# Performance work log

Hardware: AMD Instinct MI355X
Metric: run time of the kernel (lower is better)

Reference implementation:

```python
import jax, jax.numpy as jnp
import numpy as np

K_INIT = 16  # self.k from __init__

def setup_inputs() -> dict:
    key = jax.random.key(0)
    center = jax.random.normal(key, (8192, 64), dtype=jnp.float32)
    return {"center": center}

def _cdist(x):
    # Euclidean pairwise distances, matmul-based like torch.cdist(p=2).
    x2 = jnp.sum(x * x, axis=-1)  # [N]
    d2 = x2[:, None] + x2[None, :] - 2.0 * (x @ x.T)  # [N, N]
    d2 = jnp.maximum(d2, 0.0)
    # safe sqrt (grad-safe at 0; forward identical)
    d = jnp.sqrt(jnp.where(d2 > 0.0, d2, 1.0))
    return jnp.where(d2 > 0.0, d, 0.0)

def reference(center):
    n, d_feat = center.shape
    k = min(K_INIT + 1, d_feat)  # faithful to torch: min(self.k + 1, center.shape[1])
    dist = _cdist(center)  # [N, N]
    # smallest-k via top_k on negated distances
    _, indices = jax.lax.top_k(-dist, k)  # [N, k]
    neighbor_indices = indices[:, 1:]  # drop self, [N, k-1]
    mean_dists = jnp.take_along_axis(dist, neighbor_indices, axis=1).mean(axis=1)  # [N]
    logp = jax.nn.log_softmax(mean_dists, axis=0)  # = softmax(mean_dists).log()
    q = 1.0 / n
    # F.kl_div(p.log(), q, reduction='sum') = sum q * (log q - log p)
    loss = jnp.sum(q * (jnp.log(jnp.float32(q)) - logp))
    return loss
```

## Files before the change

kernel.cpp:

```cpp
#include <hip/hip_runtime.h>
#include <hip/hip_bf16.h>
#include <math.h>

#define N_PTS 8192
#define D_FEAT 64
#define KP 128
#define TPB 512
#define ROWS_B 32
#define JSPLIT 2
#define JRANGE (N_PTS / JSPLIT)
#define CHUNKS_PB (JRANGE / 32)
#define PASSES (CHUNKS_PB / 8)
#define NLIST 32

typedef __attribute__((ext_vector_type(8))) short short8v;
typedef __attribute__((ext_vector_type(16))) float f32x16;

__device__ ushort g_X2[N_PTS * KP];
__device__ float  g_x2n[N_PTS];
__device__ float  g_part[(size_t)N_PTS * NLIST * 16];
__device__ float  g_md[N_PTS];

__global__ __launch_bounds__(256) void pack_kernel(const float* __restrict__ x) {
    const int row = blockIdx.x * 256 + threadIdx.x;
    const int chunk = row >> 5, r = row & 31;
    const float4* xr = (const float4*)(x + (size_t)row * D_FEAT);
    ushort* base = g_X2 + (size_t)chunk * 4096 + r * 8;
    float norm = 0.f;
    #pragma unroll
    for (int it = 0; it < 8; ++it) {
        float4 a = xr[2 * it], b = xr[2 * it + 1];
        float vals[8] = {a.x, a.y, a.z, a.w, b.x, b.y, b.z, b.w};
        uint hi[8], lo[8];
        #pragma unroll
        for (int e = 0; e < 8; ++e) {
            float v = vals[e];
            norm += v * v;
            uint u = __float_as_uint(v);
            uint rh = (u + 0x7fffu + ((u >> 16) & 1u)) >> 16;
            hi[e] = rh;
            float l = v - __uint_as_float(rh << 16);
            uint u2 = __float_as_uint(l);
            lo[e] = (u2 + 0x7fffu + ((u2 >> 16) & 1u)) >> 16;
        }
        *(uint4*)(base + it * 256) = make_uint4(
            hi[0] | (hi[1] << 16), hi[2] | (hi[3] << 16),
            hi[4] | (hi[5] << 16), hi[6] | (hi[7] << 16));
        *(uint4*)(base + (8 + it) * 256) = make_uint4(
            lo[0] | (lo[1] << 16), lo[2] | (lo[3] << 16),
            lo[4] | (lo[5] << 16), lo[6] | (lo[7] << 16));
    }
    g_x2n[row] = norm;
}

#define CE(A, B) { float lo_ = fminf(A, B); float hi_ = fmaxf(A, B); A = lo_; B = hi_; }

__global__ __launch_bounds__(TPB, 3) void nn_kernel() {
    __shared__ float s_x2[JRANGE];
    const int t    = threadIdx.x;
    const int lane = t & 63;
    const int w    = t >> 6;
    const int il   = lane & 31;
    const int h    = lane >> 5;
    const int ib   = blockIdx.x >> 1;
    const int jslice = blockIdx.x & 1;
    const int i0   = ib * ROWS_B;
    const int c0   = jslice * CHUNKS_PB;
    const float INF = __builtin_inff();

    {
        float4* s4 = (float4*)s_x2;
        const float4* g4 = (const float4*)(g_x2n + jslice * JRANGE);
        #pragma unroll
        for (int q = 0; q < 2; ++q) s4[t + q * TPB] = g4[t + q * TPB];
    }

    const short8v* Xf = (const short8v*)g_X2;

    short8v bfr[8];
    {
        const short8v* bp = Xf + (size_t)(ib * 16 + h) * 32 + il;
        #pragma unroll
        for (int tt = 0; tt < 8; ++tt) bfr[tt] = bp[(size_t)(2 * tt) * 32];
    }
    __syncthreads();

    float t16[16];
    #pragma unroll
    for (int k = 0; k < 16; ++k) t16[k] = INF;

    const short8v* abase = Xf + (size_t)((c0 + w) * 16 + h) * 32 + il;
    #define ALOAD(dst, p) { \
        const short8v* ab_ = abase + (size_t)(p) * 8 * 16 * 32; \
        _Pragma("unroll") \
        for (int tt = 0; tt < 8; ++tt) dst[tt] = ab_[(size_t)(2 * tt) * 32]; }

    #define EPILOG(accv, p) { \
        const int cl_ = (p) * 8 + w; \
        float c[16]; \
        _Pragma("unroll") \
        for (int g = 0; g < 4; ++g) { \
            float4 xq = *(const float4*)&s_x2[cl_ * 32 + 8 * g + 4 * h]; \
            float cand[4] = {xq.x, xq.y, xq.z, xq.w}; \
            _Pragma("unroll") \
            for (int e = 0; e < 4; ++e) \
                c[4 * g + e] = fmaf(-2.f, accv[4 * g + e], cand[e]); \
        } \
         \
        CE(c[0],c[8]) CE(c[1],c[9]) CE(c[2],c[10]) CE(c[3],c[11]) \
        CE(c[4],c[12]) CE(c[5],c[13]) CE(c[6],c[14]) CE(c[7],c[15]) \
        CE(c[0],c[4]) CE(c[1],c[5]) CE(c[2],c[6]) CE(c[3],c[7]) \
        CE(c[8],c[12]) CE(c[9],c[13]) CE(c[10],c[14]) CE(c[11],c[15]) \
        CE(c[4],c[8]) CE(c[5],c[9]) CE(c[6],c[10]) CE(c[7],c[11]) \
        CE(c[0],c[2]) CE(c[1],c[3]) CE(c[4],c[6]) CE(c[5],c[7]) \
        CE(c[8],c[10]) CE(c[9],c[11]) CE(c[12],c[14]) CE(c[13],c[15]) \
        CE(c[2],c[8]) CE(c[3],c[9]) CE(c[6],c[12]) CE(c[7],c[13]) \
        CE(c[2],c[4]) CE(c[3],c[5]) CE(c[6],c[8]) CE(c[7],c[9]) \
        CE(c[10],c[12]) CE(c[11],c[13]) \
        CE(c[0],c[1]) CE(c[2],c[3]) CE(c[4],c[5]) CE(c[6],c[7]) \
        CE(c[8],c[9]) CE(c[10],c[11]) CE(c[12],c[13]) CE(c[14],c[15]) \
        CE(c[1],c[8]) CE(c[3],c[10]) CE(c[5],c[12]) CE(c[7],c[14]) \
        CE(c[1],c[4]) CE(c[3],c[6]) CE(c[5],c[8]) CE(c[7],c[10]) \
        CE(c[9],c[12]) CE(c[11],c[14]) \
        CE(c[1],c[2]) CE(c[3],c[4]) CE(c[5],c[6]) CE(c[7],c[8]) \
        CE(c[9],c[10]) CE(c[11],c[12]) CE(c[13],c[14]) \
         \
        _Pragma("unroll") \
        for (int i = 0; i < 16; ++i) t16[i] = fminf(t16[i], c[15 - i]); \
        _Pragma("unroll") \
        for (int j = 8; j > 0; j >>= 1) { \
            _Pragma("unroll") \
            for (int i = 0; i < 16; ++i) { \
                const int ix = i ^ j; \
                if (ix > i) { \
                    float lo = fminf(t16[i], t16[ix]); \
                    float hi = fmaxf(t16[i], t16[ix]); \
                    t16[i] = lo; \
                    t16[ix] = hi; \
                } \
            } \
        } }

    #define MFMA8(accv, areg) { \
        _Pragma("unroll") \
        for (int r = 0; r < 16; ++r) accv[r] = 0.f; \
        _Pragma("unroll") \
        for (int tt = 0; tt < 8; ++tt) \
            accv = __builtin_amdgcn_mfma_f32_32x32x16_bf16(areg[tt], bfr[tt], accv, 0, 0, 0); }

    short8v a0[8], a1[8];
    f32x16 acc;
    ALOAD(a0, 0);
    #pragma unroll 1
    for (int pp = 0; pp < PASSES / 2; ++pp) {
        const int p0 = 2 * pp, p1 = 2 * pp + 1;
        ALOAD(a1, p1);
        MFMA8(acc, a0);
        EPILOG(acc, p0);
        if (pp < PASSES / 2 - 1) ALOAD(a0, p1 + 1);
        MFMA8(acc, a1);
        EPILOG(acc, p1);
    }

    {
        const bool own = ((ib >> 7) == jslice) && (w == (ib & 7)) &&
                         (h == ((il >> 2) & 1));
        if (own) {
            #pragma unroll
            for (int k = 0; k < 15; ++k) t16[k] = t16[k + 1];
            t16[15] = INF;
        }
    }

    {
        const int list = jslice * 16 + w * 2 + h;
        const int row = i0 + il;
        float* dst = &g_part[((size_t)row * NLIST + list) * 16];
        *(float4*)(dst + 0)  = make_float4(t16[0],  t16[1],  t16[2],  t16[3]);
        *(float4*)(dst + 4)  = make_float4(t16[4],  t16[5],  t16[6],  t16[7]);
        *(float4*)(dst + 8)  = make_float4(t16[8],  t16[9],  t16[10], t16[11]);
        *(float4*)(dst + 12) = make_float4(t16[12], t16[13], t16[14], t16[15]);
    }
}

__global__ __launch_bounds__(512) void merge_kernel() {
    const int t = threadIdx.x, lane = t & 63, w = t >> 6;
    const int half = lane >> 5;
    const int sl = lane & 31;
    const int row = blockIdx.x * 16 + w * 2 + half;
    const float INF = __builtin_inff();

    float tl[16];
    {
        const float* src = &g_part[((size_t)row * NLIST + sl) * 16];
        float4 q0 = *(const float4*)(src + 0);
        float4 q1 = *(const float4*)(src + 4);
        float4 q2 = *(const float4*)(src + 8);
        float4 q3 = *(const float4*)(src + 12);
        tl[0] = q0.x;  tl[1] = q0.y;  tl[2] = q0.z;  tl[3] = q0.w;
        tl[4] = q1.x;  tl[5] = q1.y;  tl[6] = q1.z;  tl[7] = q1.w;
        tl[8] = q2.x;  tl[9] = q2.y;  tl[10] = q2.z; tl[11] = q2.w;
        tl[12] = q3.x; tl[13] = q3.y; tl[14] = q3.z; tl[15] = q3.w;
    }

    const float x2r = g_x2n[row];
    float sum = 0.f;
    #pragma unroll 1
    for (int it = 0; it < 16; ++it) {
        float m = tl[0]; int src = sl;
        #pragma unroll
        for (int off = 16; off > 0; off >>= 1) {
            float om = __shfl_xor(m, off);
            int os = __shfl_xor(src, off);
            if (om < m || (om == m && os < src)) { m = om; src = os; }
        }
        sum += sqrtf(fmaxf(m + x2r, 0.f));
        const bool pop = (sl == src);
        #pragma unroll
        for (int k = 0; k < 15; ++k) tl[k] = pop ? tl[k + 1] : tl[k];
        tl[15] = pop ? INF : tl[15];
    }
    if (sl == 0) g_md[row] = sum * (1.f / 16.f);
}

__global__ __launch_bounds__(1024) void loss_kernel(float* __restrict__ out) {
    __shared__ float s[1024];
    const int t = threadIdx.x;

    float m = -__builtin_inff();
    for (int j = t; j < N_PTS; j += 1024) m = fmaxf(m, g_md[j]);
    s[t] = m; __syncthreads();
    for (int off = 512; off > 0; off >>= 1) {
        if (t < off) s[t] = fmaxf(s[t], s[t + off]);
        __syncthreads();
    }
    m = s[0]; __syncthreads();

    float se = 0.f, sm = 0.f;
    for (int j = t; j < N_PTS; j += 1024) {
        float v = g_md[j];
        se += expf(v - m);
        sm += v;
    }
    s[t] = se; __syncthreads();
    for (int off = 512; off > 0; off >>= 1) {
        if (t < off) s[t] += s[t + off];
        __syncthreads();
    }
    float S = s[0]; __syncthreads();
    s[t] = sm; __syncthreads();
    for (int off = 512; off > 0; off >>= 1) {
        if (t < off) s[t] += s[t + off];
        __syncthreads();
    }
    float M = s[0];

    if (t == 0) {
        const float n = (float)N_PTS;
        out[0] = -logf(n) - M / n + (m + logf(S));
    }
}

extern "C" void kernel_launch(void* const* d_in, const int* in_sizes, int n_in,
                              void* d_out, int out_size, void* d_ws, size_t ws_size,
                              hipStream_t stream) {
    const float* x = (const float*)d_in[0];
    float* out = (float*)d_out;

    pack_kernel<<<N_PTS / 256, 256, 0, stream>>>(x);
    nn_kernel<<<(N_PTS / ROWS_B) * JSPLIT, TPB, 0, stream>>>();
    merge_kernel<<<N_PTS / 16, 512, 0, stream>>>();
    loss_kernel<<<1, 1024, 0, stream>>>(out);
}
```

Before: 67.60 us.

## Fuse top-k merge into nn kernel and drop the column split

The two-way column split and the separate merge kernel are removed. Each block now scans all 8192 columns, writes its 16 partial lists per row into shared memory, and merges them in-kernel with 16-lane shuffles. This removes the 8 MB global partial buffer round trip and one launch. The MFMA/epilogue loop is also reordered with two accumulators so one MFMA batch overlaps the previous epilogue. The cost is half as many blocks (256), which is fewer than two per CU, plus occupancy launch bounds lowered from 3 to 2, so latency hiding may suffer.

```diff
diff --git a/kernel.cpp b/kernel.cpp
--- a/kernel.cpp
+++ b/kernel.cpp
@@ -7,18 +7,14 @@
 #define KP 128
 #define TPB 512
 #define ROWS_B 32
-#define JSPLIT 2
-#define JRANGE (N_PTS / JSPLIT)
-#define CHUNKS_PB (JRANGE / 32)
-#define PASSES (CHUNKS_PB / 8)
-#define NLIST 32
+#define PASSES 32
+#define LSTRIDE 260
 
 typedef __attribute__((ext_vector_type(8))) short short8v;
 typedef __attribute__((ext_vector_type(16))) float f32x16;
 
 __device__ ushort g_X2[N_PTS * KP];
 __device__ float  g_x2n[N_PTS];
-__device__ float  g_part[(size_t)N_PTS * NLIST * 16];
 __device__ float  g_md[N_PTS];
 
 __global__ __launch_bounds__(256) void pack_kernel(const float* __restrict__ x) {
@@ -55,24 +51,22 @@
 
 #define CE(A, B) { float lo_ = fminf(A, B); float hi_ = fmaxf(A, B); A = lo_; B = hi_; }
 
-__global__ __launch_bounds__(TPB, 3) void nn_kernel() {
-    __shared__ float s_x2[JRANGE];
+__global__ __launch_bounds__(TPB, 2) void nn_kernel() {
+    __shared__ float s_mem[8320];
     const int t    = threadIdx.x;
     const int lane = t & 63;
     const int w    = t >> 6;
     const int il   = lane & 31;
     const int h    = lane >> 5;
-    const int ib   = blockIdx.x >> 1;
-    const int jslice = blockIdx.x & 1;
+    const int ib   = blockIdx.x;
     const int i0   = ib * ROWS_B;
-    const int c0   = jslice * CHUNKS_PB;
     const float INF = __builtin_inff();
 
     {
-        float4* s4 = (float4*)s_x2;
-        const float4* g4 = (const float4*)(g_x2n + jslice * JRANGE);
+        float4* s4 = (float4*)s_mem;
+        const float4* g4 = (const float4*)g_x2n;
         #pragma unroll
-        for (int q = 0; q < 2; ++q) s4[t + q * TPB] = g4[t + q * TPB];
+        for (int q = 0; q < 4; ++q) s4[t + q * TPB] = g4[t + q * TPB];
     }
 
     const short8v* Xf = (const short8v*)g_X2;
@@ -89,9 +83,9 @@
     #pragma unroll
     for (int k = 0; k < 16; ++k) t16[k] = INF;
 
-    const short8v* abase = Xf + (size_t)((c0 + w) * 16 + h) * 32 + il;
+    const short8v* abase = Xf + (size_t)(w * 16 + h) * 32 + il;
     #define ALOAD(dst, p) { \
-        const short8v* ab_ = abase + (size_t)(p) * 8 * 16 * 32; \
+        const short8v* ab_ = abase + (size_t)(p) * 4096; \
         _Pragma("unroll") \
         for (int tt = 0; tt < 8; ++tt) dst[tt] = ab_[(size_t)(2 * tt) * 32]; }
 
@@ -100,7 +94,7 @@
         float c[16]; \
         _Pragma("unroll") \
         for (int g = 0; g < 4; ++g) { \
-            float4 xq = *(const float4*)&s_x2[cl_ * 32 + 8 * g + 4 * h]; \
+            float4 xq = *(const float4*)&s_mem[cl_ * 32 + 8 * g + 4 * h]; \
             float cand[4] = {xq.x, xq.y, xq.z, xq.w}; \
             _Pragma("unroll") \
             for (int e = 0; e < 4; ++e) \
@@ -149,22 +143,22 @@
             accv = __builtin_amdgcn_mfma_f32_32x32x16_bf16(areg[tt], bfr[tt], accv, 0, 0, 0); }
 
     short8v a0[8], a1[8];
-    f32x16 acc;
+    f32x16 accA, accB;
     ALOAD(a0, 0);
+    MFMA8(accA, a0);
+    ALOAD(a1, 1);
     #pragma unroll 1
     for (int pp = 0; pp < PASSES / 2; ++pp) {
         const int p0 = 2 * pp, p1 = 2 * pp + 1;
-        ALOAD(a1, p1);
-        MFMA8(acc, a0);
-        EPILOG(acc, p0);
-        if (pp < PASSES / 2 - 1) ALOAD(a0, p1 + 1);
-        MFMA8(acc, a1);
-        EPILOG(acc, p1);
-    }
-
-    {
-        const bool own = ((ib >> 7) == jslice) && (w == (ib & 7)) &&
-                         (h == ((il >> 2) & 1));
+        MFMA8(accB, a1);
+        if (pp < PASSES / 2 - 1) ALOAD(a0, p0 + 2);
+        EPILOG(accA, p0);
+        if (pp < PASSES / 2 - 1) { ALOAD(a1, p1 + 2); MFMA8(accA, a0); }
+        EPILOG(accB, p1);
+    }
+
+    {
+        const bool own = (w == (ib & 7)) && (h == ((il >> 2) & 1));
         if (own) {
             #pragma unroll
             for (int k = 0; k < 15; ++k) t16[k] = t16[k + 1];
@@ -172,55 +166,53 @@
         }
     }
 
-    {
-        const int list = jslice * 16 + w * 2 + h;
-        const int row = i0 + il;
-        float* dst = &g_part[((size_t)row * NLIST + list) * 16];
+    __syncthreads();
+    {
+        const int list = w * 2 + h;
+        float* dst = &s_mem[il * LSTRIDE + list * 16];
         *(float4*)(dst + 0)  = make_float4(t16[0],  t16[1],  t16[2],  t16[3]);
         *(float4*)(dst + 4)  = make_float4(t16[4],  t16[5],  t16[6],  t16[7]);
         *(float4*)(dst + 8)  = make_float4(t16[8],  t16[9],  t16[10], t16[11]);
         *(float4*)(dst + 12) = make_float4(t16[12], t16[13], t16[14], t16[15]);
     }
-}
-
-__global__ __launch_bounds__(512) void merge_kernel() {
-    const int t = threadIdx.x, lane = t & 63, w = t >> 6;
-    const int half = lane >> 5;
-    const int sl = lane & 31;
-    const int row = blockIdx.x * 16 + w * 2 + half;
-    const float INF = __builtin_inff();
-
-    float tl[16];
-    {
-        const float* src = &g_part[((size_t)row * NLIST + sl) * 16];
-        float4 q0 = *(const float4*)(src + 0);
-        float4 q1 = *(const float4*)(src + 4);
-        float4 q2 = *(const float4*)(src + 8);
-        float4 q3 = *(const float4*)(src + 12);
-        tl[0] = q0.x;  tl[1] = q0.y;  tl[2] = q0.z;  tl[3] = q0.w;
-        tl[4] = q1.x;  tl[5] = q1.y;  tl[6] = q1.z;  tl[7] = q1.w;
-        tl[8] = q2.x;  tl[9] = q2.y;  tl[10] = q2.z; tl[11] = q2.w;
-        tl[12] = q3.x; tl[13] = q3.y; tl[14] = q3.z; tl[15] = q3.w;
-    }
-
-    const float x2r = g_x2n[row];
-    float sum = 0.f;
-    #pragma unroll 1
-    for (int it = 0; it < 16; ++it) {
-        float m = tl[0]; int src = sl;
-        #pragma unroll
-        for (int off = 16; off > 0; off >>= 1) {
-            float om = __shfl_xor(m, off);
-            int os = __shfl_xor(src, off);
-            if (om < m || (om == m && os < src)) { m = om; src = os; }
-        }
-        sum += sqrtf(fmaxf(m + x2r, 0.f));
-        const bool pop = (sl == src);
-        #pragma unroll
-        for (int k = 0; k < 15; ++k) tl[k] = pop ? tl[k + 1] : tl[k];
-        tl[15] = pop ? INF : tl[15];
-    }
-    if (sl == 0) g_md[row] = sum * (1.f / 16.f);
+    __syncthreads();
+
+    {
+        const int q  = lane >> 4;
+        const int sl = lane & 15;
+        const int r  = w * 4 + q;
+        const int row = i0 + r;
+        float tl[16];
+        {
+            const float* src = &s_mem[r * LSTRIDE + sl * 16];
+            float4 q0 = *(const float4*)(src + 0);
+            float4 q1 = *(const float4*)(src + 4);
+            float4 q2 = *(const float4*)(src + 8);
+            float4 q3 = *(const float4*)(src + 12);
+            tl[0]=q0.x; tl[1]=q0.y; tl[2]=q0.z; tl[3]=q0.w;
+            tl[4]=q1.x; tl[5]=q1.y; tl[6]=q1.z; tl[7]=q1.w;
+            tl[8]=q2.x; tl[9]=q2.y; tl[10]=q2.z; tl[11]=q2.w;
+            tl[12]=q3.x; tl[13]=q3.y; tl[14]=q3.z; tl[15]=q3.w;
+        }
+        const float x2r = g_x2n[row];
+        float sum = 0.f;
+        #pragma unroll 1
+        for (int it = 0; it < 16; ++it) {
+            float m = tl[0]; int src = sl;
+            #pragma unroll
+            for (int off = 8; off > 0; off >>= 1) {
+                float om = __shfl_xor(m, off);
+                int os = __shfl_xor(src, off);
+                if (om < m || (om == m && os < src)) { m = om; src = os; }
+            }
+            sum += sqrtf(fmaxf(m + x2r, 0.f));
+            const bool pop = (sl == src);
+            #pragma unroll
+            for (int k = 0; k < 15; ++k) tl[k] = pop ? tl[k + 1] : tl[k];
+            tl[15] = pop ? INF : tl[15];
+        }
+        if (sl == 0) g_md[row] = sum * (1.f / 16.f);
+    }
 }
 
 __global__ __launch_bounds__(1024) void loss_kernel(float* __restrict__ out) {
@@ -268,7 +260,6 @@
     float* out = (float*)d_out;
 
     pack_kernel<<<N_PTS / 256, 256, 0, stream>>>(x);
-    nn_kernel<<<(N_PTS / ROWS_B) * JSPLIT, TPB, 0, stream>>>();
-    merge_kernel<<<N_PTS / 16, 512, 0, stream>>>();
+    nn_kernel<<<N_PTS / ROWS_B, TPB, 0, stream>>>();
     loss_kernel<<<1, 1024, 0, stream>>>(out);
 }
```

New measurement: 61.75 us. 1.09x faster.
